# Performance work log

Measured on AMD Instinct MI355X. Metric: run time of the kernel, lower is better.

The kernel has to match this reference:

```python
import jax, jax.numpy as jnp
import numpy as np

V, E, S, B, N = 100000, 300, 1024, 64, 5
H = [512, 256, 128]

def setup_inputs() -> dict:
    key = jax.random.key(0)
    ks = jax.random.split(key, 10)
    x = jax.random.randint(ks[0], (B, S), 0, V, dtype=jnp.int32)
    # lengths must be >= n for valid n-gram counts (original assumes this)
    lengths = jax.random.randint(ks[1], (B,), N, S + 1, dtype=jnp.int32)
    sc = lambda f: 1.0 / np.sqrt(f)
    table = jax.random.normal(ks[2], (V, E), dtype=jnp.float32)
    W_slide = jax.random.uniform(ks[3], (N * E, H[0]), jnp.float32, -sc(N * E), sc(N * E))
    b_slide = jax.random.uniform(ks[4], (H[0],), jnp.float32, -sc(N * E), sc(N * E))
    W1 = jax.random.uniform(ks[5], (H[0], H[1]), jnp.float32, -sc(H[0]), sc(H[0]))
    b1 = jax.random.uniform(ks[6], (H[1],), jnp.float32, -sc(H[0]), sc(H[0]))
    W2 = jax.random.uniform(ks[7], (H[1], H[2]), jnp.float32, -sc(H[1]), sc(H[1]))
    b2 = jax.random.uniform(ks[8], (H[2],), jnp.float32, -sc(H[1]), sc(H[1]))
    return {"x": x, "lengths": lengths, "table": table, "W_slide": W_slide,
            "b_slide": b_slide, "W1": W1, "b1": b1, "W2": W2, "b2": b2}

def reference(x, lengths, table, W_slide, b_slide, W1, b1, W2, b2):
    n = N
    Wn = S - (n - 1)  # number of sliding windows per sequence
    emb = table[x]  # [B, S, E]
    # gather sliding windows: [B, Wn, n, E] -> [B, Wn, n*E]
    idx = jnp.arange(Wn)[:, None] + jnp.arange(n)[None, :]
    win = emb[:, idx].reshape(B, Wn, n * E)
    h = win @ W_slide + b_slide              # [B, Wn, H0]
    h = jax.nn.relu(h @ W1 + b1)             # [B, Wn, H1]
    h = jax.nn.relu(h @ W2 + b2)             # [B, Wn, H2]
    # ragged mean over valid n-gram positions per sample
    valid = (lengths - (n - 1)).astype(h.dtype)           # [B]
    mask = (jnp.arange(Wn)[None, :] < (lengths - (n - 1))[:, None]).astype(h.dtype)
    pooled = jnp.einsum('bwh,bw->bh', h, mask) / valid[:, None]
    return pooled
```

## Files before the change

kernel.cpp:

```cpp
#include <hip/hip_runtime.h>

#define B_N    64
#define S_LEN  1024
#define EMB    300
#define EMB_P  304
#define NGRAM  5
#define WPAD   1024
#define MTOT   (B_N * WPAD)
#define K1P    1536
#define H0     512
#define H1D    256
#define H2D    128
#define NK1    (K1P / 32)
#define NSTEP1 (K1P / 64)

#define GATHER_BLOCKS ((MTOT * 38) / 256)
#define WPREP_THREADS (H0 * K1P + H1D * H0 + H2D * H1D)
#define WPREP_BLOCKS  ((WPREP_THREADS + 255) / 256)

typedef _Float16 half8 __attribute__((ext_vector_type(8)));
typedef float  floatx4 __attribute__((ext_vector_type(4)));

typedef const __attribute__((address_space(1))) void* gptr_t;
typedef __attribute__((address_space(3))) void* sptr_t;

__device__ __forceinline__ void gload16(const void* g, void* s) {
  __builtin_amdgcn_global_load_lds((gptr_t)g, (sptr_t)s, 16, 0, 0);
}

__global__ void gatherk(const int* __restrict__ x,
                        const int* __restrict__ lengths,
                        const float* __restrict__ table,
                        _Float16* __restrict__ emb,
                        float* __restrict__ out) {
  const int bid = blockIdx.x;
  if (bid < 32) out[bid * 256 + threadIdx.x] = 0.0f;
  int tid = bid * 256 + threadIdx.x;
  int tok = tid / 38;
  int c   = tid - tok * 38;
  int valid = lengths[tok >> 10] - (NGRAM - 1);
  int limit = ((valid + 127) & ~127) + (NGRAM - 1);
  if ((tok & 1023) >= limit) return;
  int e = c << 3;
  const float* row = table + (size_t)x[tok] * EMB + e;
  float4 v0 = *(const float4*)row;
  float4 v1 = make_float4(0.0f, 0.0f, 0.0f, 0.0f);
  if (e + 4 < EMB) v1 = *(const float4*)(row + 4);
  union { half8 h8; _Float16 h[8]; } u;
  u.h[0] = (_Float16)v0.x; u.h[1] = (_Float16)v0.y;
  u.h[2] = (_Float16)v0.z; u.h[3] = (_Float16)v0.w;
  u.h[4] = (_Float16)v1.x; u.h[5] = (_Float16)v1.y;
  u.h[6] = (_Float16)v1.z; u.h[7] = (_Float16)v1.w;
  *(half8*)(emb + (size_t)tok * EMB_P + e) = u.h8;
}

__global__ void wprepk(const int* __restrict__ lengths,
                       const float* __restrict__ Ws,
                       const float* __restrict__ W1,
                       const float* __restrict__ W2,
                       _Float16* __restrict__ Bf1,
                       _Float16* __restrict__ Bf2,
                       _Float16* __restrict__ Bf3,
                       int* __restrict__ meta) {
  __shared__ int sN[64], sP[65], sN6[64], sP6[65];
  const int bid = blockIdx.x;
  if (bid < WPREP_BLOCKS) {
    int tid = bid * 256 + threadIdx.x;
    const int NS = H0 * K1P;
    const int N1 = H1D * H0;
    const int N2 = H2D * H1D;
    if (tid < NS) {
      int n = tid & 511, k = tid >> 9;
      float v = 0.0f;
      if (k < NGRAM * EMB_P) {
        int tn = k / EMB_P, e = k - tn * EMB_P;
        if (e < EMB) v = Ws[(size_t)(tn * EMB + e) * H0 + n];
      }
      int idx = ((((n >> 4) * NK1 + (k >> 5)) << 6) + (((k >> 3) & 3) << 4) + (n & 15)) * 8 + (k & 7);
      Bf1[idx] = (_Float16)v;
    } else if (tid < NS + N1) {
      int t = tid - NS;
      int n = t & 255, k = t >> 8;
      float v = W1[(size_t)k * H1D + n];
      int idx = ((((n >> 4) * 16 + (k >> 5)) << 6) + (((k >> 3) & 3) << 4) + (n & 15)) * 8 + (k & 7);
      Bf2[idx] = (_Float16)v;
    } else if (tid < NS + N1 + N2) {
      int t = tid - (NS + N1);
      int n = t & 127, k = t >> 7;
      float v = W2[(size_t)k * H2D + n];
      int idx = ((((n >> 4) * 8 + (k >> 5)) << 6) + (((k >> 3) & 3) << 4) + (n & 15)) * 8 + (k & 7);
      Bf3[idx] = (_Float16)v;
    }
  } else {
    int t = threadIdx.x;
    if (t < 64) {
      int valid = lengths[t] - (NGRAM - 1);
      sN[t]  = (valid + 127) >> 7;
      sN6[t] = (valid + 63) >> 6;
    }
    __syncthreads();
    if (t == 0) {
      int s = 0, s6 = 0;
      for (int i = 0; i < 64; i++) {
        sP[i] = s;  s  += sN[i];
        sP6[i] = s6; s6 += sN6[i];
      }
      meta[0] = s; meta[1] = s6;
    }
    __syncthreads();
    if (t < 64) {
      int base = sP[t], n = sN[t];
      for (int i = 0; i < n; i++) meta[8 + base + i] = (t << 3) + i;
      int b6 = sP6[t], n6 = sN6[t];
      for (int i = 0; i < n6; i++) meta[520 + b6 + i] = (t << 4) + i;
    }
  }
}

__global__ __launch_bounds__(256, 3)
void gemm1(const _Float16* __restrict__ A, const _Float16* __restrict__ Bf,
           const float* __restrict__ bias, _Float16* __restrict__ Cf,
           const int* __restrict__ meta) {
  __shared__ _Float16 sA[2][128 * 64];

  const int nLive4 = meta[0] << 2;
  const int xcd = blockIdx.x & 7, bi = blockIdx.x >> 3;
  const int q = nLive4 >> 3, r = nLive4 & 7;
  if (bi >= q + (xcd < r ? 1 : 0)) return;
  const int L = xcd * q + (xcd < r ? xcd : r) + bi;
  const int mt = meta[8 + (L >> 2)], nt = L & 3;

  const int tid  = threadIdx.x;
  const int wave = tid >> 6, lane = tid & 63;
  const int wr   = wave >> 1, wc = wave & 1;
  const int quad = lane >> 4, l16 = lane & 15;

  const long mBase = (long)mt << 7;
  const int  nBase = nt << 7;

  const int srow0  = (wave << 3) + (lane >> 3);
  const int schunk = lane & 7;
  const _Float16* aG[4];
  int sOff[4];
#pragma unroll
  for (int p = 0; p < 4; p++) {
    int row = (p << 5) + srow0;
    int c   = schunk ^ (row & 7);
    aG[p]   = A + (mBase + row) * EMB_P + (c << 3);
    sOff[p] = (row << 6) + (schunk << 3);
  }

  const _Float16* bG[4];
#pragma unroll
  for (int j = 0; j < 4; j++)
    bG[j] = Bf + (((size_t)((nBase >> 4) + (wc << 2) + j) * NK1) << 9) + (lane << 3);

  int aOff[2][4];
#pragma unroll
  for (int s = 0; s < 2; s++)
#pragma unroll
    for (int i = 0; i < 4; i++) {
      int rr   = (wr << 6) + (i << 4) + l16;
      int slot = ((s << 2) + quad) ^ (l16 & 7);
      aOff[s][i] = (rr << 6) + (slot << 3);
    }

  floatx4 acc[4][4] = {};

#pragma unroll
  for (int p = 0; p < 4; p++) gload16(aG[p], &sA[0][sOff[p]]);
  half8 bCur[2][4], bNxt[2][4];
#pragma unroll
  for (int s = 0; s < 2; s++)
#pragma unroll
    for (int j = 0; j < 4; j++)
      bCur[s][j] = *(const half8*)(bG[j] + ((size_t)s << 9));

#pragma unroll 2
  for (int kk = 0; kk < NSTEP1; kk++) {
    const int cur = kk & 1;
    __syncthreads();
    if (kk + 1 < NSTEP1) {
      const int ko = (kk + 1) << 6;
#pragma unroll
      for (int p = 0; p < 4; p++) gload16(aG[p] + ko, &sA[cur ^ 1][sOff[p]]);
#pragma unroll
      for (int s = 0; s < 2; s++)
#pragma unroll
        for (int j = 0; j < 4; j++)
          bNxt[s][j] = *(const half8*)(bG[j] + (size_t)((((kk + 1) << 1) + s) << 9));
    }
#pragma unroll
    for (int s = 0; s < 2; s++) {
      half8 aFr[4];
#pragma unroll
      for (int i = 0; i < 4; i++)
        aFr[i] = *(const half8*)(&sA[cur][aOff[s][i]]);
#pragma unroll
      for (int i = 0; i < 4; i++)
#pragma unroll
        for (int j = 0; j < 4; j++)
          acc[i][j] = __builtin_amdgcn_mfma_f32_16x16x32_f16(aFr[i], bCur[s][j], acc[i][j], 0, 0, 0);
    }
#pragma unroll
    for (int s = 0; s < 2; s++)
#pragma unroll
      for (int j = 0; j < 4; j++)
        bCur[s][j] = bNxt[s][j];
  }

  __syncthreads();
  _Float16* cs = &sA[0][0];
#pragma unroll
  for (int j = 0; j < 4; j++) {
    int cl = (wc << 6) + (j << 4) + l16;
    float bv = bias[nBase + cl];
    int ksl = cl >> 5;
    int sub_hi = ((cl >> 3) & 3) << 4;
    int c7 = cl & 7;
#pragma unroll
    for (int i = 0; i < 4; i++) {
      int m16l = (wr << 2) + i;
#pragma unroll
      for (int rr = 0; rr < 4; rr++) {
        int ml = (quad << 2) + rr;
        cs[(((m16l << 2) + ksl) << 9) + ((sub_hi + ml) << 3) + c7] =
            (_Float16)(acc[i][j][rr] + bv);
      }
    }
  }
  __syncthreads();
#pragma unroll
  for (int it = 0; it < 8; it++) {
    int cid = (it << 2) + wave;
    int m16l = cid >> 2, ksl = cid & 3;
    size_t g = ((size_t)(((mt << 3) + m16l) * 16 + (nt << 2) + ksl) << 9) + (lane << 3);
    *(half8*)(Cf + g) = *(const half8*)(cs + (cid << 9) + (lane << 3));
  }
}

__global__ __launch_bounds__(256, 3)
void gemm23(const _Float16* __restrict__ Af, const _Float16* __restrict__ B2,
            const _Float16* __restrict__ B3, const float* __restrict__ bias1,
            const float* __restrict__ bias2, float* __restrict__ out,
            const int* __restrict__ lengths, const int* __restrict__ meta) {
  __shared__ _Float16 sH[16384];

  if ((int)blockIdx.x >= meta[1]) return;
  const int mt = meta[520 + blockIdx.x];

  const int tid  = threadIdx.x;
  const int wave = tid >> 6, lane = tid & 63;
  const int wc   = wave;
  const int quad = lane >> 4, l16 = lane & 15;

  const int b = mt >> 4;
  const int validw = lengths[b] - (NGRAM - 1);

  const _Float16* aB = Af + (((size_t)(mt << 2) * 16) << 9) + (lane << 3);
  const _Float16* bB = B2 + ((size_t)wc << 15) + (lane << 3);

  floatx4 acc2[4][4] = {};
  half8 aP[4], bP[4], aQ[4], bQ[4];

  auto loadA = [&](half8* d, int kk) {
#pragma unroll
    for (int i = 0; i < 4; i++)
      d[i] = *(const half8*)(aB + ((size_t)kk << 9) + ((size_t)i << 13));
  };
  auto loadB = [&](half8* d, int kk) {
#pragma unroll
    for (int j = 0; j < 4; j++)
      d[j] = *(const half8*)(bB + ((size_t)kk << 9) + ((size_t)j << 13));
  };
  auto mfmaStep = [&](const half8* aF, const half8* bF) {
    __builtin_amdgcn_s_setprio(1);
#pragma unroll
    for (int i = 0; i < 4; i++)
#pragma unroll
      for (int j = 0; j < 4; j++)
        acc2[i][j] = __builtin_amdgcn_mfma_f32_16x16x32_f16(aF[i], bF[j], acc2[i][j], 0, 0, 0);
    __builtin_amdgcn_s_setprio(0);
  };

  loadA(aP, 0); loadB(bP, 0);
#pragma unroll
  for (int kk = 0; kk < 16; kk += 2) {
    loadA(aQ, kk + 1); loadB(bQ, kk + 1);
    mfmaStep(aP, bP);
    if (kk + 2 < 16) { loadA(aP, kk + 2); loadB(bP, kk + 2); }
    mfmaStep(aQ, bQ);
  }

#pragma unroll
  for (int j = 0; j < 4; j++) {
    int n = (wc << 6) + (j << 4) + l16;
    float bv = bias1[n];
    int ks = n >> 5;
    int sub_hi = ((n >> 3) & 3) << 4;
    int c7 = n & 7;
#pragma unroll
    for (int i = 0; i < 4; i++) {
#pragma unroll
      for (int rr = 0; rr < 4; rr++) {
        int ml = (quad << 2) + rr;
        sH[(((i << 3) + ks) << 9) + ((sub_hi + ml) << 3) + c7] =
            (_Float16)fmaxf(acc2[i][j][rr] + bv, 0.0f);
      }
    }
  }
  __syncthreads();

  const _Float16* b3R[2];
#pragma unroll
  for (int j = 0; j < 2; j++)
    b3R[j] = B3 + (((size_t)((wc << 1) + j) * 8) << 9) + (lane << 3);

  floatx4 acc3[4][2] = {};
#pragma unroll
  for (int ks = 0; ks < 8; ks++) {
    half8 aF[4], bF[2];
#pragma unroll
    for (int i = 0; i < 4; i++)
      aF[i] = *(const half8*)(sH + (((i << 3) + ks) << 9) + (lane << 3));
#pragma unroll
    for (int j = 0; j < 2; j++) bF[j] = *(const half8*)(b3R[j] + ((size_t)ks << 9));
    __builtin_amdgcn_s_setprio(1);
#pragma unroll
    for (int i = 0; i < 4; i++)
#pragma unroll
      for (int j = 0; j < 2; j++)
        acc3[i][j] = __builtin_amdgcn_mfma_f32_16x16x32_f16(aF[i], bF[j], acc3[i][j], 0, 0, 0);
    __builtin_amdgcn_s_setprio(0);
  }

  float inv = 1.0f / (float)validw;
  int wBase = (mt & 15) << 6;
#pragma unroll
  for (int j = 0; j < 2; j++) {
    int col = (wc << 5) + (j << 4) + l16;
    float bv = bias2[col];
    float p = 0.0f;
#pragma unroll
    for (int i = 0; i < 4; i++) {
#pragma unroll
      for (int rr = 0; rr < 4; rr++) {
        int w = wBase + (i << 4) + (quad << 2) + rr;
        float v = fmaxf(acc3[i][j][rr] + bv, 0.0f);
        p += (w < validw) ? v : 0.0f;
      }
    }
    p *= inv;
    p += __shfl_xor(p, 16, 64);
    p += __shfl_xor(p, 32, 64);
    if (quad == 0) atomicAdd(out + b * H2D + col, p);
  }
}

extern "C" void kernel_launch(void* const* d_in, const int* in_sizes, int n_in,
                              void* d_out, int out_size, void* d_ws, size_t ws_size,
                              hipStream_t stream) {
  const int*   x       = (const int*)d_in[0];
  const int*   lengths = (const int*)d_in[1];
  const float* table   = (const float*)d_in[2];
  const float* W_slide = (const float*)d_in[3];
  const float* b_slide = (const float*)d_in[4];
  const float* W1      = (const float*)d_in[5];
  const float* b1      = (const float*)d_in[6];
  const float* W2      = (const float*)d_in[7];
  const float* b2      = (const float*)d_in[8];
  float* out = (float*)d_out;

  _Float16* ws  = (_Float16*)d_ws;
  _Float16* emb = ws;
  _Float16* Bf1 = emb + (size_t)MTOT * EMB_P + 4096;
  _Float16* Bf2 = Bf1 + (size_t)H0 * K1P;
  _Float16* Bf3 = Bf2 + (size_t)H1D * H0;
  _Float16* h1f = Bf3 + (size_t)H2D * H1D;
  int*      meta = (int*)(h1f + (size_t)MTOT * H0);

  gatherk<<<GATHER_BLOCKS, 256, 0, stream>>>(x, lengths, table, emb, out);
  wprepk<<<WPREP_BLOCKS + 1, 256, 0, stream>>>(lengths, W_slide, W1, W2,
                                               Bf1, Bf2, Bf3, meta);
  gemm1<<<(MTOT / 128) * (H0 / 128), 256, 0, stream>>>(emb, Bf1, b_slide, h1f, meta);
  gemm23<<<MTOT / 64, 256, 0, stream>>>(h1f, Bf2, Bf3, b1, b2, out, lengths, meta);
}
```

Before: 272.5 us.

## Stage gemm1 B tiles through LDS and merge prep kernels into one launch

The first GEMM no longer loads B fragments straight from global memory into registers. Each block now copies its B tile into a double-buffered LDS array with async global_load_lds, and waves read their fragments from LDS. The gather and weight-prep kernels become one launch, and gemm1 is split into two launches, each covering half of the XCD partitions. The extra 32KB of LDS per block drops the occupancy hint from 3 to 2. The second gemm1 launch adds overhead and may serialise work that previously ran in one grid.

```diff
diff --git a/kernel.cpp b/kernel.cpp
--- a/kernel.cpp
+++ b/kernel.cpp
@@ -28,44 +28,41 @@
   __builtin_amdgcn_global_load_lds((gptr_t)g, (sptr_t)s, 16, 0, 0);
 }
 
-__global__ void gatherk(const int* __restrict__ x,
-                        const int* __restrict__ lengths,
-                        const float* __restrict__ table,
-                        _Float16* __restrict__ emb,
-                        float* __restrict__ out) {
-  const int bid = blockIdx.x;
-  if (bid < 32) out[bid * 256 + threadIdx.x] = 0.0f;
-  int tid = bid * 256 + threadIdx.x;
-  int tok = tid / 38;
-  int c   = tid - tok * 38;
-  int valid = lengths[tok >> 10] - (NGRAM - 1);
-  int limit = ((valid + 127) & ~127) + (NGRAM - 1);
-  if ((tok & 1023) >= limit) return;
-  int e = c << 3;
-  const float* row = table + (size_t)x[tok] * EMB + e;
-  float4 v0 = *(const float4*)row;
-  float4 v1 = make_float4(0.0f, 0.0f, 0.0f, 0.0f);
-  if (e + 4 < EMB) v1 = *(const float4*)(row + 4);
-  union { half8 h8; _Float16 h[8]; } u;
-  u.h[0] = (_Float16)v0.x; u.h[1] = (_Float16)v0.y;
-  u.h[2] = (_Float16)v0.z; u.h[3] = (_Float16)v0.w;
-  u.h[4] = (_Float16)v1.x; u.h[5] = (_Float16)v1.y;
-  u.h[6] = (_Float16)v1.z; u.h[7] = (_Float16)v1.w;
-  *(half8*)(emb + (size_t)tok * EMB_P + e) = u.h8;
-}
-
-__global__ void wprepk(const int* __restrict__ lengths,
-                       const float* __restrict__ Ws,
-                       const float* __restrict__ W1,
-                       const float* __restrict__ W2,
-                       _Float16* __restrict__ Bf1,
-                       _Float16* __restrict__ Bf2,
-                       _Float16* __restrict__ Bf3,
-                       int* __restrict__ meta) {
+__global__ void prep_kernel(const int* __restrict__ x,
+                            const int* __restrict__ lengths,
+                            const float* __restrict__ table,
+                            _Float16* __restrict__ emb,
+                            float* __restrict__ out,
+                            const float* __restrict__ Ws,
+                            const float* __restrict__ W1,
+                            const float* __restrict__ W2,
+                            _Float16* __restrict__ Bf1,
+                            _Float16* __restrict__ Bf2,
+                            _Float16* __restrict__ Bf3,
+                            int* __restrict__ meta) {
   __shared__ int sN[64], sP[65], sN6[64], sP6[65];
   const int bid = blockIdx.x;
-  if (bid < WPREP_BLOCKS) {
+  if (bid < GATHER_BLOCKS) {
+    if (bid < 32) out[bid * 256 + threadIdx.x] = 0.0f;
     int tid = bid * 256 + threadIdx.x;
+    int tok = tid / 38;
+    int c   = tid - tok * 38;
+    int valid = lengths[tok >> 10] - (NGRAM - 1);
+    int limit = ((valid + 127) & ~127) + (NGRAM - 1);
+    if ((tok & 1023) >= limit) return;
+    int e = c << 3;
+    const float* row = table + (size_t)x[tok] * EMB + e;
+    float4 v0 = *(const float4*)row;
+    float4 v1 = make_float4(0.0f, 0.0f, 0.0f, 0.0f);
+    if (e + 4 < EMB) v1 = *(const float4*)(row + 4);
+    union { half8 h8; _Float16 h[8]; } u;
+    u.h[0] = (_Float16)v0.x; u.h[1] = (_Float16)v0.y;
+    u.h[2] = (_Float16)v0.z; u.h[3] = (_Float16)v0.w;
+    u.h[4] = (_Float16)v1.x; u.h[5] = (_Float16)v1.y;
+    u.h[6] = (_Float16)v1.z; u.h[7] = (_Float16)v1.w;
+    *(half8*)(emb + (size_t)tok * EMB_P + e) = u.h8;
+  } else if (bid < GATHER_BLOCKS + WPREP_BLOCKS) {
+    int tid = (bid - GATHER_BLOCKS) * 256 + threadIdx.x;
     const int NS = H0 * K1P;
     const int N1 = H1D * H0;
     const int N2 = H2D * H1D;
@@ -102,7 +99,7 @@
     if (t == 0) {
       int s = 0, s6 = 0;
       for (int i = 0; i < 64; i++) {
-        sP[i] = s;  s  += sN[i];
+        sP[i] = s;   s  += sN[i];
         sP6[i] = s6; s6 += sN6[i];
       }
       meta[0] = s; meta[1] = s6;
@@ -117,14 +114,15 @@
   }
 }
 
-__global__ __launch_bounds__(256, 3)
+__global__ __launch_bounds__(256, 2)
 void gemm1(const _Float16* __restrict__ A, const _Float16* __restrict__ Bf,
            const float* __restrict__ bias, _Float16* __restrict__ Cf,
-           const int* __restrict__ meta) {
+           const int* __restrict__ meta, int xcdBase) {
   __shared__ _Float16 sA[2][128 * 64];
+  __shared__ _Float16 sB[2][128 * 64];
 
   const int nLive4 = meta[0] << 2;
-  const int xcd = blockIdx.x & 7, bi = blockIdx.x >> 3;
+  const int xcd = xcdBase + (blockIdx.x & 3), bi = blockIdx.x >> 2;
   const int q = nLive4 >> 3, r = nLive4 & 7;
   if (bi >= q + (xcd < r ? 1 : 0)) return;
   const int L = xcd * q + (xcd < r ? xcd : r) + bi;
@@ -141,19 +139,26 @@
   const int srow0  = (wave << 3) + (lane >> 3);
   const int schunk = lane & 7;
   const _Float16* aG[4];
-  int sOff[4];
+  int sOffA[4];
 #pragma unroll
   for (int p = 0; p < 4; p++) {
     int row = (p << 5) + srow0;
     int c   = schunk ^ (row & 7);
     aG[p]   = A + (mBase + row) * EMB_P + (c << 3);
-    sOff[p] = (row << 6) + (schunk << 3);
-  }
-
-  const _Float16* bG[4];
-#pragma unroll
-  for (int j = 0; j < 4; j++)
-    bG[j] = Bf + (((size_t)((nBase >> 4) + (wc << 2) + j) * NK1) << 9) + (lane << 3);
+    sOffA[p] = (row << 6) + (schunk << 3);
+  }
+
+  const _Float16* bSrc[4];
+  int sOffB[4];
+#pragma unroll
+  for (int p = 0; p < 4; p++) {
+    int idx   = (p << 8) + tid;
+    int n16l  = idx >> 7;
+    int s     = (idx >> 6) & 1;
+    int lane_s = idx & 63;
+    bSrc[p]  = Bf + (((size_t)((nBase >> 4) + n16l) * NK1 + s) << 9) + (lane_s << 3);
+    sOffB[p] = idx << 3;
+  }
 
   int aOff[2][4];
 #pragma unroll
@@ -164,49 +169,47 @@
       int slot = ((s << 2) + quad) ^ (l16 & 7);
       aOff[s][i] = (rr << 6) + (slot << 3);
     }
+  int bOff[2][4];
+#pragma unroll
+  for (int s = 0; s < 2; s++)
+#pragma unroll
+    for (int j = 0; j < 4; j++)
+      bOff[s][j] = (((((wc << 2) + j) << 1) + s) << 9) + (lane << 3);
 
   floatx4 acc[4][4] = {};
 
 #pragma unroll
-  for (int p = 0; p < 4; p++) gload16(aG[p], &sA[0][sOff[p]]);
-  half8 bCur[2][4], bNxt[2][4];
-#pragma unroll
-  for (int s = 0; s < 2; s++)
-#pragma unroll
-    for (int j = 0; j < 4; j++)
-      bCur[s][j] = *(const half8*)(bG[j] + ((size_t)s << 9));
+  for (int p = 0; p < 4; p++) gload16(aG[p], &sA[0][sOffA[p]]);
+#pragma unroll
+  for (int p = 0; p < 4; p++) gload16(bSrc[p], &sB[0][sOffB[p]]);
 
 #pragma unroll 2
   for (int kk = 0; kk < NSTEP1; kk++) {
     const int cur = kk & 1;
     __syncthreads();
     if (kk + 1 < NSTEP1) {
-      const int ko = (kk + 1) << 6;
-#pragma unroll
-      for (int p = 0; p < 4; p++) gload16(aG[p] + ko, &sA[cur ^ 1][sOff[p]]);
-#pragma unroll
-      for (int s = 0; s < 2; s++)
-#pragma unroll
-        for (int j = 0; j < 4; j++)
-          bNxt[s][j] = *(const half8*)(bG[j] + (size_t)((((kk + 1) << 1) + s) << 9));
+      const int koA = (kk + 1) << 6;
+      const size_t koB = (size_t)(kk + 1) << 10;
+#pragma unroll
+      for (int p = 0; p < 4; p++) gload16(aG[p] + koA, &sA[cur ^ 1][sOffA[p]]);
+#pragma unroll
+      for (int p = 0; p < 4; p++) gload16(bSrc[p] + koB, &sB[cur ^ 1][sOffB[p]]);
     }
 #pragma unroll
     for (int s = 0; s < 2; s++) {
-      half8 aFr[4];
+      half8 aFr[4], bFr[4];
 #pragma unroll
       for (int i = 0; i < 4; i++)
         aFr[i] = *(const half8*)(&sA[cur][aOff[s][i]]);
 #pragma unroll
+      for (int j = 0; j < 4; j++)
+        bFr[j] = *(const half8*)(&sB[cur][bOff[s][j]]);
+#pragma unroll
       for (int i = 0; i < 4; i++)
 #pragma unroll
         for (int j = 0; j < 4; j++)
-          acc[i][j] = __builtin_amdgcn_mfma_f32_16x16x32_f16(aFr[i], bCur[s][j], acc[i][j], 0, 0, 0);
-    }
-#pragma unroll
-    for (int s = 0; s < 2; s++)
-#pragma unroll
-      for (int j = 0; j < 4; j++)
-        bCur[s][j] = bNxt[s][j];
+          acc[i][j] = __builtin_amdgcn_mfma_f32_16x16x32_f16(aFr[i], bFr[j], acc[i][j], 0, 0, 0);
+    }
   }
 
   __syncthreads();
@@ -379,9 +382,9 @@
   _Float16* h1f = Bf3 + (size_t)H2D * H1D;
   int*      meta = (int*)(h1f + (size_t)MTOT * H0);
 
-  gatherk<<<GATHER_BLOCKS, 256, 0, stream>>>(x, lengths, table, emb, out);
-  wprepk<<<WPREP_BLOCKS + 1, 256, 0, stream>>>(lengths, W_slide, W1, W2,
-                                               Bf1, Bf2, Bf3, meta);
-  gemm1<<<(MTOT / 128) * (H0 / 128), 256, 0, stream>>>(emb, Bf1, b_slide, h1f, meta);
+  prep_kernel<<<GATHER_BLOCKS + WPREP_BLOCKS + 1, 256, 0, stream>>>(
+      x, lengths, table, emb, out, W_slide, W1, W2, Bf1, Bf2, Bf3, meta);
+  gemm1<<<1024, 256, 0, stream>>>(emb, Bf1, b_slide, h1f, meta, 0);
+  gemm1<<<1024, 256, 0, stream>>>(emb, Bf1, b_slide, h1f, meta, 4);
   gemm23<<<MTOT / 64, 256, 0, stream>>>(h1f, Bf2, Bf3, b1, b2, out, lengths, meta);
 }
```

After: 292.9 us. 1.08x slower.
